# Optimization experiments

Measured on AMD Instinct MI355X. Metric: run time of the kernel, lower is better.

Reference implementation:

```python
import jax, jax.numpy as jnp
import numpy as np

IMG, P, C, E = 256, 16, 3, 200
N = (IMG // P) ** 2          # 256 patches
NUM_MASKED = int(N * 0.75)   # 192
PATCH_ELEMS = C * P * P      # 768


def setup_inputs() -> dict:
    key = jax.random.key(0)
    ks = jax.random.split(key, 10)
    B = 128
    x = jax.random.normal(ks[0], (B, C, IMG, IMG), dtype=jnp.float32)
    perm = jax.random.permutation(ks[1], N).astype(jnp.int32)
    conv_w = jax.random.normal(ks[2], (E, C, P, P), dtype=jnp.float32) * 0.02
    conv_b = jnp.zeros((E,), dtype=jnp.float32)
    pos_embed = jax.random.normal(ks[3], (1, N, E), dtype=jnp.float32) * 0.02
    mask_token = jnp.zeros((1, E), dtype=jnp.float32)
    W_enc = jax.random.normal(ks[4], (E, E), dtype=jnp.float32) * (1.0 / np.sqrt(E))
    b_enc = jnp.zeros((E,), dtype=jnp.float32)
    W_dec = jax.random.normal(ks[5], (E, PATCH_ELEMS), dtype=jnp.float32) * (1.0 / np.sqrt(E))
    b_dec = jnp.zeros((PATCH_ELEMS,), dtype=jnp.float32)
    return {"x": x, "conv_w": conv_w, "conv_b": conv_b, "pos_embed": pos_embed,
            "mask_token": mask_token, "W_enc": W_enc, "b_enc": b_enc,
            "W_dec": W_dec, "b_dec": b_dec, "perm": perm}


def _patchify(x):
    # [B,C,H,W] -> [B, N, C*P*P], row-major patch order (matches conv stride=P then flatten)
    B = x.shape[0]
    g = IMG // P
    x = x.reshape(B, C, g, P, g, P)           # B C gh P gw P
    x = x.transpose(0, 2, 4, 1, 3, 5)         # B gh gw C P P
    return x.reshape(B, g * g, C * P * P)


def _fold(patches):
    # [B, N, C*P*P] -> [B,C,H,W]; idx iterates rows (i) outer, cols (j) inner
    B = patches.shape[0]
    g = IMG // P
    p = patches.reshape(B, g, g, C, P, P)
    return p.transpose(0, 3, 1, 4, 2, 5).reshape(B, C, IMG, IMG)


def reference(x, conv_w, conv_b, pos_embed, mask_token, W_enc, b_enc, W_dec, b_dec, perm):
    masked_idx = perm[:NUM_MASKED]
    unmasked_idx = perm[NUM_MASKED:]
    # patch embed (Conv2d k=P, stride=P == linear over flattened patches)
    patches = _patchify(x)                                   # [B,N,768]
    w_flat = conv_w.reshape(E, -1)                           # [E, 768]
    emb = jnp.einsum('bnp,ep->bne', patches, w_flat) + conv_b + pos_embed  # [B,N,E]
    visible = emb[:, unmasked_idx, :]                        # [B, N-192, E]
    encoded = jnp.einsum('bne,ef->bnf', visible, W_enc) + b_enc
    B = x.shape[0]
    full = jnp.zeros((B, N, E), dtype=x.dtype)
    full = full.at[:, unmasked_idx, :].set(encoded)
    full = full.at[:, masked_idx, :].set(jnp.broadcast_to(mask_token, (B, NUM_MASKED, E)))
    full = full + pos_embed
    dec = jnp.einsum('bne,ep->bnp', full, W_dec) + b_dec     # [B,N,768]
    img = _fold(dec)                                         # [B,C,H,W]
    return img, masked_idx
```

## Files before the change

### kernel.cpp

```cpp
#include <hip/hip_runtime.h>

typedef __attribute__((ext_vector_type(8))) __bf16 bf16x8;
typedef __attribute__((ext_vector_type(4))) float f32x4;

constexpr int Bsz   = 128;
constexpr int EE    = 200;
constexpr int EP    = 256;
constexpr int KP    = 224;
constexpr int NN    = 256;
constexpr int NMASK = 192;
constexpr int NVIS  = 64;
constexpr int PE    = 768;
constexpr int M1    = Bsz * NVIS;
constexpr int M3    = M1 + NMASK;
constexpr long IMG_ELEMS = (long)Bsz * 3 * 256 * 256;

__global__ __launch_bounds__(256) void k_prep(
    const float* __restrict__ pos, const float* __restrict__ wflat,
    const float* __restrict__ Wenc, const float* __restrict__ Wdec,
    const float* __restrict__ conv_b, const float* __restrict__ b_enc,
    const float* __restrict__ mask_token, const int* __restrict__ perm,
    float* __restrict__ posP, __bf16* __restrict__ W1t,
    __bf16* __restrict__ W2t, __bf16* __restrict__ W3t,
    float* __restrict__ cbp, float* __restrict__ bep,
    __bf16* __restrict__ full, float* __restrict__ out_idx)
{
    int blk = blockIdx.x, t = threadIdx.x;
    if (blk < 256) {
        posP[blk * 256 + t] = (t < EE) ? pos[blk * EE + t] : 0.f;
        return;
    }
    blk -= 256;
    if (blk < 768) {
        int e = blk / 3, k = (blk % 3) * 256 + t;
        W1t[e * 768 + k] = (e < EE) ? (__bf16)wflat[e * 768 + k] : (__bf16)0.f;
        return;
    }
    blk -= 768;
    if (blk < 256) {
        if (t < KP) W2t[blk * KP + t] =
            (blk < EE && t < EE) ? (__bf16)Wenc[t * EE + blk] : (__bf16)0.f;
        return;
    }
    blk -= 256;
    if (blk < 768) {
        if (t < KP) W3t[blk * KP + t] =
            (t < EE) ? (__bf16)Wdec[t * PE + blk] : (__bf16)0.f;
        return;
    }
    blk -= 768;
    if (blk < NMASK) {
        int n = perm[blk];
        full[(M1 + blk) * EP + t] =
            (t < EE) ? (__bf16)(mask_token[t] + pos[n * EE + t]) : (__bf16)0.f;
        return;
    }
    cbp[t] = (t < EE) ? conv_b[t] : 0.f;
    bep[t] = (t < EE) ? b_enc[t] : 0.f;
    if (t < NMASK) out_idx[t] = (float)perm[t];
}

__global__ __launch_bounds__(256) void k_gemm1(
    const float* __restrict__ x, const __bf16* __restrict__ W1t,
    const float* __restrict__ cbp, const float* __restrict__ posP,
    const int* __restrict__ perm, __bf16* __restrict__ visible)
{
    __shared__ __bf16 As[64][40];
    __shared__ __bf16 Bs[64][40];
    const int t = threadIdx.x;
    const int m0 = blockIdx.y * 64, e0 = blockIdx.x * 64;
    const int row = t >> 2, chunk = t & 3;
    const int lane = t & 63, wid = t >> 6;
    const int wr = wid >> 1, wc = wid & 1;
    const int quad = lane >> 4, lid = lane & 15;

    const int am = m0 + row;
    const int an = perm[NMASK + (am & 63)];
    const int abase = (am >> 6) * 196608 + (an >> 4) * 4096 + (an & 15) * 16;

    f32x4 acc[2][2] = {};

    for (int k0 = 0; k0 < PE; k0 += 32) {
        int k = k0 + chunk * 8;
        int c = k >> 8, py = (k >> 4) & 15, px = k & 15;
        const float* ap = x + abase + c * 65536 + py * 256 + px;
        float4 a0 = *(const float4*)ap;
        float4 a1 = *(const float4*)(ap + 4);
        bf16x8 av;
        av[0] = (__bf16)a0.x; av[1] = (__bf16)a0.y; av[2] = (__bf16)a0.z; av[3] = (__bf16)a0.w;
        av[4] = (__bf16)a1.x; av[5] = (__bf16)a1.y; av[6] = (__bf16)a1.z; av[7] = (__bf16)a1.w;
        *(bf16x8*)&As[row][chunk * 8] = av;
        *(int4*)&Bs[row][chunk * 8] = *(const int4*)&W1t[(e0 + row) * 768 + k];
        __syncthreads();
        #pragma unroll
        for (int i = 0; i < 2; ++i) {
            bf16x8 af = *(const bf16x8*)&As[wr * 32 + i * 16 + lid][quad * 8];
            #pragma unroll
            for (int j = 0; j < 2; ++j) {
                bf16x8 bfv = *(const bf16x8*)&Bs[wc * 32 + j * 16 + lid][quad * 8];
                acc[i][j] = __builtin_amdgcn_mfma_f32_16x16x32_bf16(af, bfv, acc[i][j], 0, 0, 0);
            }
        }
        __syncthreads();
    }

    #pragma unroll
    for (int i = 0; i < 2; ++i) {
        int mb = m0 + wr * 32 + i * 16 + quad * 4;
        #pragma unroll
        for (int j = 0; j < 2; ++j) {
            int e = e0 + wc * 32 + j * 16 + lid;
            #pragma unroll
            for (int r = 0; r < 4; ++r) {
                int m = mb + r;
                int n = perm[NMASK + (m & 63)];
                float v = acc[i][j][r] + cbp[e] + posP[n * 256 + e];
                visible[m * EP + e] = (__bf16)v;
            }
        }
    }
}

__global__ __launch_bounds__(256) void k_gemm2(
    const __bf16* __restrict__ visible, const __bf16* __restrict__ W2t,
    const float* __restrict__ bep, const float* __restrict__ posP,
    const int* __restrict__ perm, __bf16* __restrict__ full)
{
    __shared__ __bf16 As[64][40];
    __shared__ __bf16 Bs[64][40];
    const int t = threadIdx.x;
    const int m0 = blockIdx.y * 64, e0 = blockIdx.x * 64;
    const int row = t >> 2, chunk = t & 3;
    const int lane = t & 63, wid = t >> 6;
    const int wr = wid >> 1, wc = wid & 1;
    const int quad = lane >> 4, lid = lane & 15;

    f32x4 acc[2][2] = {};

    for (int k0 = 0; k0 < KP; k0 += 32) {
        int k = k0 + chunk * 8;
        *(int4*)&As[row][chunk * 8] = *(const int4*)&visible[(m0 + row) * EP + k];
        *(int4*)&Bs[row][chunk * 8] = *(const int4*)&W2t[(e0 + row) * KP + k];
        __syncthreads();
        #pragma unroll
        for (int i = 0; i < 2; ++i) {
            bf16x8 af = *(const bf16x8*)&As[wr * 32 + i * 16 + lid][quad * 8];
            #pragma unroll
            for (int j = 0; j < 2; ++j) {
                bf16x8 bfv = *(const bf16x8*)&Bs[wc * 32 + j * 16 + lid][quad * 8];
                acc[i][j] = __builtin_amdgcn_mfma_f32_16x16x32_bf16(af, bfv, acc[i][j], 0, 0, 0);
            }
        }
        __syncthreads();
    }

    #pragma unroll
    for (int i = 0; i < 2; ++i) {
        int mb = m0 + wr * 32 + i * 16 + quad * 4;
        #pragma unroll
        for (int j = 0; j < 2; ++j) {
            int e = e0 + wc * 32 + j * 16 + lid;
            #pragma unroll
            for (int r = 0; r < 4; ++r) {
                int m = mb + r;
                int n = perm[NMASK + (m & 63)];
                float v = acc[i][j][r] + bep[e] + posP[n * 256 + e];
                full[m * EP + e] = (__bf16)v;
            }
        }
    }
}

__global__ __launch_bounds__(256) void k_gemm3(
    const __bf16* __restrict__ full, const __bf16* __restrict__ W3t,
    const float* __restrict__ bdec, const int* __restrict__ perm,
    float* __restrict__ img, float* __restrict__ dec_masked)
{
    __shared__ __bf16 As[64][40];
    __shared__ __bf16 Bs[64][40];
    const int t = threadIdx.x;
    const int m0 = blockIdx.y * 64, e0 = blockIdx.x * 64;
    const int row = t >> 2, chunk = t & 3;
    const int lane = t & 63, wid = t >> 6;
    const int wr = wid >> 1, wc = wid & 1;
    const int quad = lane >> 4, lid = lane & 15;

    f32x4 acc[2][2] = {};

    for (int k0 = 0; k0 < KP; k0 += 32) {
        int k = k0 + chunk * 8;
        *(int4*)&As[row][chunk * 8] = *(const int4*)&full[(m0 + row) * EP + k];
        *(int4*)&Bs[row][chunk * 8] = *(const int4*)&W3t[(e0 + row) * KP + k];
        __syncthreads();
        #pragma unroll
        for (int i = 0; i < 2; ++i) {
            bf16x8 af = *(const bf16x8*)&As[wr * 32 + i * 16 + lid][quad * 8];
            #pragma unroll
            for (int j = 0; j < 2; ++j) {
                bf16x8 bfv = *(const bf16x8*)&Bs[wc * 32 + j * 16 + lid][quad * 8];
                acc[i][j] = __builtin_amdgcn_mfma_f32_16x16x32_bf16(af, bfv, acc[i][j], 0, 0, 0);
            }
        }
        __syncthreads();
    }

    const bool vis = (m0 < M1);
    #pragma unroll
    for (int i = 0; i < 2; ++i) {
        int mb = m0 + wr * 32 + i * 16 + quad * 4;
        #pragma unroll
        for (int j = 0; j < 2; ++j) {
            int e = e0 + wc * 32 + j * 16 + lid;
            int c = e >> 8, py = (e >> 4) & 15, px = e & 15;
            #pragma unroll
            for (int r = 0; r < 4; ++r) {
                int m = mb + r;
                float v = acc[i][j][r] + bdec[e];
                if (vis) {
                    int b = m >> 6;
                    int n = perm[NMASK + (m & 63)];
                    img[(long)(b * 3 + c) * 65536 + ((n >> 4) * 16 + py) * 256
                        + (n & 15) * 16 + px] = v;
                } else {
                    dec_masked[(m - M1) * PE + e] = v;
                }
            }
        }
    }
}

__global__ __launch_bounds__(192) void k_foldmask(
    const float* __restrict__ dec_masked, const int* __restrict__ perm,
    float* __restrict__ img)
{
    const int i = blockIdx.x;
    const int b = blockIdx.y;
    const int n = perm[i];
    const int t = threadIdx.x;
    float4 v = *(const float4*)&dec_masked[i * PE + t * 4];
    int p = t * 4;
    int c = p >> 8, py = (p >> 4) & 15, px = p & 15;
    *(float4*)&img[(long)(b * 3 + c) * 65536 + ((n >> 4) * 16 + py) * 256
                   + (n & 15) * 16 + px] = v;
}

extern "C" void kernel_launch(void* const* d_in, const int* in_sizes, int n_in,
                              void* d_out, int out_size, void* d_ws, size_t ws_size,
                              hipStream_t stream)
{
    const float* x          = (const float*)d_in[0];
    const float* conv_w     = (const float*)d_in[1];
    const float* conv_b     = (const float*)d_in[2];
    const float* pos        = (const float*)d_in[3];
    const float* mask_token = (const float*)d_in[4];
    const float* W_enc      = (const float*)d_in[5];
    const float* b_enc      = (const float*)d_in[6];
    const float* W_dec      = (const float*)d_in[7];
    const float* b_dec      = (const float*)d_in[8];
    const int*   perm       = (const int*)d_in[9];
    float* out = (float*)d_out;

    __bf16* visible = (__bf16*)d_ws;
    __bf16* full    = visible + M1 * EP;
    __bf16* W1t     = full + M3 * EP;
    __bf16* W2t     = W1t + 256 * 768;
    __bf16* W3t     = W2t + 256 * KP;
    float*  posP    = (float*)(W3t + 768 * KP);
    float*  cbp     = posP + 256 * 256;
    float*  bep     = cbp + 256;
    float*  decm    = bep + 256;

    k_prep<<<256 + 768 + 256 + 768 + NMASK + 1, 256, 0, stream>>>(
        pos, conv_w, W_enc, W_dec, conv_b, b_enc, mask_token, perm,
        posP, W1t, W2t, W3t, cbp, bep, full, out + IMG_ELEMS);
    k_gemm1<<<dim3(4, 128), 256, 0, stream>>>(x, W1t, cbp, posP, perm, visible);
    k_gemm2<<<dim3(4, 128), 256, 0, stream>>>(visible, W2t, bep, posP, perm, full);
    k_gemm3<<<dim3(12, 131), 256, 0, stream>>>(full, W3t, b_dec, perm, out, decm);
    k_foldmask<<<dim3(NMASK, Bsz), 192, 0, stream>>>(decm, perm, out);
}
```

Before: 244.6 us.

## Fuse three GEMMs into one megakernel keeping intermediates in LDS

Replaces the three separate GEMM kernels with one kernel in which each 512-thread block takes 32 visible rows through patch-embed, encoder and decoder GEMMs, keeping the activations in shared memory instead of round-tripping through global memory. Extra blocks compute the batch-independent masked-token decoder rows. Weights are read straight from global/L2 with no LDS staging, and the fold-mask kernel now writes 8 batches per block. This removes two launches and the intermediate traffic, at the cost of only 262 blocks and per-wave global weight reads, which may limit occupancy.

```diff
diff --git a/kernel.cpp b/kernel.cpp
--- a/kernel.cpp
+++ b/kernel.cpp
@@ -15,6 +15,15 @@
 constexpr int M3    = M1 + NMASK;
 constexpr long IMG_ELEMS = (long)Bsz * 3 * 256 * 256;
 
+constexpr int VBLK = 256;
+constexpr int ASTR = 776;
+constexpr int TSTR = 264;
+constexpr int FOFF = 32 * TSTR;
+
+__device__ __forceinline__ f32x4 mfma16(bf16x8 a, bf16x8 b, f32x4 c) {
+    return __builtin_amdgcn_mfma_f32_16x16x32_bf16(a, b, c, 0, 0, 0);
+}
+
 __global__ __launch_bounds__(256) void k_prep(
     const float* __restrict__ pos, const float* __restrict__ wflat,
     const float* __restrict__ Wenc, const float* __restrict__ Wdec,
@@ -60,170 +69,170 @@
     if (t < NMASK) out_idx[t] = (float)perm[t];
 }
 
-__global__ __launch_bounds__(256) void k_gemm1(
+__global__ __launch_bounds__(512) void k_mega(
     const float* __restrict__ x, const __bf16* __restrict__ W1t,
-    const float* __restrict__ cbp, const float* __restrict__ posP,
-    const int* __restrict__ perm, __bf16* __restrict__ visible)
-{
-    __shared__ __bf16 As[64][40];
-    __shared__ __bf16 Bs[64][40];
-    const int t = threadIdx.x;
-    const int m0 = blockIdx.y * 64, e0 = blockIdx.x * 64;
-    const int row = t >> 2, chunk = t & 3;
+    const __bf16* __restrict__ W2t, const __bf16* __restrict__ W3t,
+    const float* __restrict__ cbp, const float* __restrict__ bep,
+    const float* __restrict__ posP, const float* __restrict__ bdec,
+    const int* __restrict__ perm, const __bf16* __restrict__ fullg,
+    float* __restrict__ img, float* __restrict__ dec_masked)
+{
+    __shared__ __bf16 smem[32 * ASTR];
+    __bf16* As    = smem;
+    __bf16* vis_t = smem;
+    __bf16* ful_t = smem + FOFF;
+    __shared__ int nidx[32];
+
+    const int t    = threadIdx.x;
+    const int bid  = blockIdx.x;
     const int lane = t & 63, wid = t >> 6;
-    const int wr = wid >> 1, wc = wid & 1;
     const int quad = lane >> 4, lid = lane & 15;
 
-    const int am = m0 + row;
-    const int an = perm[NMASK + (am & 63)];
-    const int abase = (am >> 6) * 196608 + (an >> 4) * 4096 + (an & 15) * 16;
-
-    f32x4 acc[2][2] = {};
-
-    for (int k0 = 0; k0 < PE; k0 += 32) {
-        int k = k0 + chunk * 8;
-        int c = k >> 8, py = (k >> 4) & 15, px = k & 15;
-        const float* ap = x + abase + c * 65536 + py * 256 + px;
-        float4 a0 = *(const float4*)ap;
-        float4 a1 = *(const float4*)(ap + 4);
-        bf16x8 av;
-        av[0] = (__bf16)a0.x; av[1] = (__bf16)a0.y; av[2] = (__bf16)a0.z; av[3] = (__bf16)a0.w;
-        av[4] = (__bf16)a1.x; av[5] = (__bf16)a1.y; av[6] = (__bf16)a1.z; av[7] = (__bf16)a1.w;
-        *(bf16x8*)&As[row][chunk * 8] = av;
-        *(int4*)&Bs[row][chunk * 8] = *(const int4*)&W1t[(e0 + row) * 768 + k];
+    if (bid >= VBLK) {
+        const int mb = bid - VBLK;
+        #pragma unroll
+        for (int it = 0; it < 2; ++it) {
+            int cchunk = t + it * 512;
+            int row = cchunk >> 5, col = (cchunk & 31) * 8;
+            *(int4*)&ful_t[row * TSTR + col] =
+                *(const int4*)&fullg[(M1 + mb * 32 + row) * EP + col];
+        }
         __syncthreads();
+        f32x4 acc[2][6] = {};
+        const int p0w = wid * 96;
+        for (int k0 = 0; k0 < KP; k0 += 32) {
+            bf16x8 a0 = *(const bf16x8*)&ful_t[lid * TSTR + k0 + quad * 8];
+            bf16x8 a1 = *(const bf16x8*)&ful_t[(16 + lid) * TSTR + k0 + quad * 8];
+            #pragma unroll
+            for (int j = 0; j < 6; ++j) {
+                bf16x8 bv = *(const bf16x8*)&W3t[(p0w + j * 16 + lid) * KP + k0 + quad * 8];
+                acc[0][j] = mfma16(a0, bv, acc[0][j]);
+                acc[1][j] = mfma16(a1, bv, acc[1][j]);
+            }
+        }
+        #pragma unroll
+        for (int j = 0; j < 6; ++j) {
+            const int p = p0w + j * 16 + lid;
+            const float bd = bdec[p];
+            #pragma unroll
+            for (int i = 0; i < 2; ++i) {
+                const int r0 = mb * 32 + i * 16 + quad * 4;
+                #pragma unroll
+                for (int r = 0; r < 4; ++r)
+                    dec_masked[(r0 + r) * PE + p] = acc[i][j][r] + bd;
+            }
+        }
+        return;
+    }
+
+    const int m0 = bid * 32;
+    if (t < 32) nidx[t] = perm[NMASK + (m0 & 63) + t];
+
+    {
+        const int row = t >> 4;
+        const int m = m0 + row;
+        const int n = perm[NMASK + (m & 63)];
+        const int abase = (m >> 6) * 196608 + (n >> 4) * 4096 + (n & 15) * 16;
+        #pragma unroll
+        for (int it = 0; it < 6; ++it) {
+            int k = (t & 15) * 8 + it * 128;
+            int c = k >> 8, py = (k >> 4) & 15, px = k & 15;
+            const float* ap = x + abase + c * 65536 + py * 256 + px;
+            float4 a0 = *(const float4*)ap;
+            float4 a1 = *(const float4*)(ap + 4);
+            bf16x8 av;
+            av[0] = (__bf16)a0.x; av[1] = (__bf16)a0.y; av[2] = (__bf16)a0.z; av[3] = (__bf16)a0.w;
+            av[4] = (__bf16)a1.x; av[5] = (__bf16)a1.y; av[6] = (__bf16)a1.z; av[7] = (__bf16)a1.w;
+            *(bf16x8*)&As[row * ASTR + k] = av;
+        }
+    }
+    __syncthreads();
+
+    const int e0w = wid * 32;
+    f32x4 acc1[2][2] = {};
+    for (int k0 = 0; k0 < 768; k0 += 32) {
+        bf16x8 a0 = *(const bf16x8*)&As[lid * ASTR + k0 + quad * 8];
+        bf16x8 a1 = *(const bf16x8*)&As[(16 + lid) * ASTR + k0 + quad * 8];
+        #pragma unroll
+        for (int j = 0; j < 2; ++j) {
+            bf16x8 bv = *(const bf16x8*)&W1t[(e0w + j * 16 + lid) * 768 + k0 + quad * 8];
+            acc1[0][j] = mfma16(a0, bv, acc1[0][j]);
+            acc1[1][j] = mfma16(a1, bv, acc1[1][j]);
+        }
+    }
+    __syncthreads();
+
+    #pragma unroll
+    for (int i = 0; i < 2; ++i) {
+        const int mloc = i * 16 + quad * 4;
+        #pragma unroll
+        for (int j = 0; j < 2; ++j) {
+            const int e = e0w + j * 16 + lid;
+            const float cb = cbp[e];
+            #pragma unroll
+            for (int r = 0; r < 4; ++r) {
+                const int ml = mloc + r;
+                vis_t[ml * TSTR + e] =
+                    (__bf16)(acc1[i][j][r] + cb + posP[nidx[ml] * 256 + e]);
+            }
+        }
+    }
+    __syncthreads();
+
+    f32x4 acc2[2][2] = {};
+    for (int k0 = 0; k0 < KP; k0 += 32) {
+        bf16x8 a0 = *(const bf16x8*)&vis_t[lid * TSTR + k0 + quad * 8];
+        bf16x8 a1 = *(const bf16x8*)&vis_t[(16 + lid) * TSTR + k0 + quad * 8];
+        #pragma unroll
+        for (int j = 0; j < 2; ++j) {
+            bf16x8 bv = *(const bf16x8*)&W2t[(e0w + j * 16 + lid) * KP + k0 + quad * 8];
+            acc2[0][j] = mfma16(a0, bv, acc2[0][j]);
+            acc2[1][j] = mfma16(a1, bv, acc2[1][j]);
+        }
+    }
+    #pragma unroll
+    for (int i = 0; i < 2; ++i) {
+        const int mloc = i * 16 + quad * 4;
+        #pragma unroll
+        for (int j = 0; j < 2; ++j) {
+            const int e = e0w + j * 16 + lid;
+            const float be = bep[e];
+            #pragma unroll
+            for (int r = 0; r < 4; ++r) {
+                const int ml = mloc + r;
+                ful_t[ml * TSTR + e] =
+                    (__bf16)(acc2[i][j][r] + be + posP[nidx[ml] * 256 + e]);
+            }
+        }
+    }
+    __syncthreads();
+
+    f32x4 acc3[2][6] = {};
+    const int p0w = wid * 96;
+    for (int k0 = 0; k0 < KP; k0 += 32) {
+        bf16x8 a0 = *(const bf16x8*)&ful_t[lid * TSTR + k0 + quad * 8];
+        bf16x8 a1 = *(const bf16x8*)&ful_t[(16 + lid) * TSTR + k0 + quad * 8];
+        #pragma unroll
+        for (int j = 0; j < 6; ++j) {
+            bf16x8 bv = *(const bf16x8*)&W3t[(p0w + j * 16 + lid) * KP + k0 + quad * 8];
+            acc3[0][j] = mfma16(a0, bv, acc3[0][j]);
+            acc3[1][j] = mfma16(a1, bv, acc3[1][j]);
+        }
+    }
+    const int bimg = m0 >> 6;
+    #pragma unroll
+    for (int j = 0; j < 6; ++j) {
+        const int p = p0w + j * 16 + lid;
+        const int c = p >> 8, py = (p >> 4) & 15, px = p & 15;
+        const float bd = bdec[p];
+        const long obase = (long)(bimg * 3 + c) * 65536 + py * 256 + px;
         #pragma unroll
         for (int i = 0; i < 2; ++i) {
-            bf16x8 af = *(const bf16x8*)&As[wr * 32 + i * 16 + lid][quad * 8];
-            #pragma unroll
-            for (int j = 0; j < 2; ++j) {
-                bf16x8 bfv = *(const bf16x8*)&Bs[wc * 32 + j * 16 + lid][quad * 8];
-                acc[i][j] = __builtin_amdgcn_mfma_f32_16x16x32_bf16(af, bfv, acc[i][j], 0, 0, 0);
-            }
-        }
-        __syncthreads();
-    }
-
-    #pragma unroll
-    for (int i = 0; i < 2; ++i) {
-        int mb = m0 + wr * 32 + i * 16 + quad * 4;
-        #pragma unroll
-        for (int j = 0; j < 2; ++j) {
-            int e = e0 + wc * 32 + j * 16 + lid;
+            const int mloc = i * 16 + quad * 4;
             #pragma unroll
             for (int r = 0; r < 4; ++r) {
-                int m = mb + r;
-                int n = perm[NMASK + (m & 63)];
-                float v = acc[i][j][r] + cbp[e] + posP[n * 256 + e];
-                visible[m * EP + e] = (__bf16)v;
-            }
-        }
-    }
-}
-
-__global__ __launch_bounds__(256) void k_gemm2(
-    const __bf16* __restrict__ visible, const __bf16* __restrict__ W2t,
-    const float* __restrict__ bep, const float* __restrict__ posP,
-    const int* __restrict__ perm, __bf16* __restrict__ full)
-{
-    __shared__ __bf16 As[64][40];
-    __shared__ __bf16 Bs[64][40];
-    const int t = threadIdx.x;
-    const int m0 = blockIdx.y * 64, e0 = blockIdx.x * 64;
-    const int row = t >> 2, chunk = t & 3;
-    const int lane = t & 63, wid = t >> 6;
-    const int wr = wid >> 1, wc = wid & 1;
-    const int quad = lane >> 4, lid = lane & 15;
-
-    f32x4 acc[2][2] = {};
-
-    for (int k0 = 0; k0 < KP; k0 += 32) {
-        int k = k0 + chunk * 8;
-        *(int4*)&As[row][chunk * 8] = *(const int4*)&visible[(m0 + row) * EP + k];
-        *(int4*)&Bs[row][chunk * 8] = *(const int4*)&W2t[(e0 + row) * KP + k];
-        __syncthreads();
-        #pragma unroll
-        for (int i = 0; i < 2; ++i) {
-            bf16x8 af = *(const bf16x8*)&As[wr * 32 + i * 16 + lid][quad * 8];
-            #pragma unroll
-            for (int j = 0; j < 2; ++j) {
-                bf16x8 bfv = *(const bf16x8*)&Bs[wc * 32 + j * 16 + lid][quad * 8];
-                acc[i][j] = __builtin_amdgcn_mfma_f32_16x16x32_bf16(af, bfv, acc[i][j], 0, 0, 0);
-            }
-        }
-        __syncthreads();
-    }
-
-    #pragma unroll
-    for (int i = 0; i < 2; ++i) {
-        int mb = m0 + wr * 32 + i * 16 + quad * 4;
-        #pragma unroll
-        for (int j = 0; j < 2; ++j) {
-            int e = e0 + wc * 32 + j * 16 + lid;
-            #pragma unroll
-            for (int r = 0; r < 4; ++r) {
-                int m = mb + r;
-                int n = perm[NMASK + (m & 63)];
-                float v = acc[i][j][r] + bep[e] + posP[n * 256 + e];
-                full[m * EP + e] = (__bf16)v;
-            }
-        }
-    }
-}
-
-__global__ __launch_bounds__(256) void k_gemm3(
-    const __bf16* __restrict__ full, const __bf16* __restrict__ W3t,
-    const float* __restrict__ bdec, const int* __restrict__ perm,
-    float* __restrict__ img, float* __restrict__ dec_masked)
-{
-    __shared__ __bf16 As[64][40];
-    __shared__ __bf16 Bs[64][40];
-    const int t = threadIdx.x;
-    const int m0 = blockIdx.y * 64, e0 = blockIdx.x * 64;
-    const int row = t >> 2, chunk = t & 3;
-    const int lane = t & 63, wid = t >> 6;
-    const int wr = wid >> 1, wc = wid & 1;
-    const int quad = lane >> 4, lid = lane & 15;
-
-    f32x4 acc[2][2] = {};
-
-    for (int k0 = 0; k0 < KP; k0 += 32) {
-        int k = k0 + chunk * 8;
-        *(int4*)&As[row][chunk * 8] = *(const int4*)&full[(m0 + row) * EP + k];
-        *(int4*)&Bs[row][chunk * 8] = *(const int4*)&W3t[(e0 + row) * KP + k];
-        __syncthreads();
-        #pragma unroll
-        for (int i = 0; i < 2; ++i) {
-            bf16x8 af = *(const bf16x8*)&As[wr * 32 + i * 16 + lid][quad * 8];
-            #pragma unroll
-            for (int j = 0; j < 2; ++j) {
-                bf16x8 bfv = *(const bf16x8*)&Bs[wc * 32 + j * 16 + lid][quad * 8];
-                acc[i][j] = __builtin_amdgcn_mfma_f32_16x16x32_bf16(af, bfv, acc[i][j], 0, 0, 0);
-            }
-        }
-        __syncthreads();
-    }
-
-    const bool vis = (m0 < M1);
-    #pragma unroll
-    for (int i = 0; i < 2; ++i) {
-        int mb = m0 + wr * 32 + i * 16 + quad * 4;
-        #pragma unroll
-        for (int j = 0; j < 2; ++j) {
-            int e = e0 + wc * 32 + j * 16 + lid;
-            int c = e >> 8, py = (e >> 4) & 15, px = e & 15;
-            #pragma unroll
-            for (int r = 0; r < 4; ++r) {
-                int m = mb + r;
-                float v = acc[i][j][r] + bdec[e];
-                if (vis) {
-                    int b = m >> 6;
-                    int n = perm[NMASK + (m & 63)];
-                    img[(long)(b * 3 + c) * 65536 + ((n >> 4) * 16 + py) * 256
-                        + (n & 15) * 16 + px] = v;
-                } else {
-                    dec_masked[(m - M1) * PE + e] = v;
-                }
+                const int n = nidx[mloc + r];
+                img[obase + (n >> 4) * 4096 + (n & 15) * 16] = acc3[i][j][r] + bd;
             }
         }
     }
@@ -233,15 +242,17 @@
     const float* __restrict__ dec_masked, const int* __restrict__ perm,
     float* __restrict__ img)
 {
-    const int i = blockIdx.x;
-    const int b = blockIdx.y;
-    const int n = perm[i];
-    const int t = threadIdx.x;
+    const int i  = blockIdx.x;
+    const int b0 = blockIdx.y * 8;
+    const int n  = perm[i];
+    const int t  = threadIdx.x;
     float4 v = *(const float4*)&dec_masked[i * PE + t * 4];
     int p = t * 4;
     int c = p >> 8, py = (p >> 4) & 15, px = p & 15;
-    *(float4*)&img[(long)(b * 3 + c) * 65536 + ((n >> 4) * 16 + py) * 256
-                   + (n & 15) * 16 + px] = v;
+    const long base = (long)c * 65536 + (n >> 4) * 4096 + (n & 15) * 16 + py * 256 + px;
+    #pragma unroll
+    for (int bb = 0; bb < 8; ++bb)
+        *(float4*)&img[(long)(b0 + bb) * 3 * 65536 + base] = v;
 }
 
 extern "C" void kernel_launch(void* const* d_in, const int* in_sizes, int n_in,
@@ -273,8 +284,7 @@
     k_prep<<<256 + 768 + 256 + 768 + NMASK + 1, 256, 0, stream>>>(
         pos, conv_w, W_enc, W_dec, conv_b, b_enc, mask_token, perm,
         posP, W1t, W2t, W3t, cbp, bep, full, out + IMG_ELEMS);
-    k_gemm1<<<dim3(4, 128), 256, 0, stream>>>(x, W1t, cbp, posP, perm, visible);
-    k_gemm2<<<dim3(4, 128), 256, 0, stream>>>(visible, W2t, bep, posP, perm, full);
-    k_gemm3<<<dim3(12, 131), 256, 0, stream>>>(full, W3t, b_dec, perm, out, decm);
-    k_foldmask<<<dim3(NMASK, Bsz), 192, 0, stream>>>(decm, perm, out);
-}
+    k_mega<<<VBLK + NMASK / 32, 512, 0, stream>>>(
+        x, W1t, W2t, W3t, cbp, bep, posP, b_dec, perm, full, out, decm);
+    k_foldmask<<<dim3(NMASK, Bsz / 8), 192, 0, stream>>>(decm, perm, out);
+}
```

Result: faster. 235.9 us (-3.6%).
